# Kernel tuning notes

Hardware: AMD Instinct MI355X
Metric: run time of the kernel (lower is better)

The kernel has to match this reference:

```python
import jax, jax.numpy as jnp
import numpy as np

B, N, D, H = 2, 2048, 1024, 16
DH = D // H


def setup_inputs() -> dict:
    key = jax.random.key(0)
    ks = jax.random.split(key, 5)
    s = 0.02
    return {
        "x": jax.random.normal(ks[0], (B, N, D), dtype=jnp.float32),
        "Wq": jax.random.normal(ks[1], (D, D), dtype=jnp.float32) * s,
        "Wk": jax.random.normal(ks[2], (D, D), dtype=jnp.float32) * s,
        "Wv": jax.random.normal(ks[3], (D, D), dtype=jnp.float32) * s,
        "Wo": jax.random.normal(ks[4], (D, D), dtype=jnp.float32) * s,
        "bo": jnp.zeros((D,), dtype=jnp.float32),
    }


def reference(x, Wq, Wk, Wv, Wo, bo):
    b, n, d = x.shape
    # linear projections (torch Linear: y = x @ W.T), split into heads -> [b,h,n,dh]
    def proj(W):
        return jnp.einsum('bnd,ed->bne', x, W).reshape(b, n, H, DH).transpose(0, 2, 1, 3)
    q, k, v = proj(Wq), proj(Wk), proj(Wv)
    scores = jnp.einsum('bhqd,bhkd->bhqk', q, k)  # [b,h,n,n]
    causal = jnp.triu(jnp.ones((n, n), dtype=bool), k=1)
    scores = jnp.where(causal, -jnp.inf, scores)
    # NOTE: module scales by 1/sqrt(num_key_tokens), not 1/sqrt(d_head)
    w = jax.nn.softmax(scores / jnp.sqrt(jnp.float32(n)), axis=-1)
    ctx = jnp.einsum('bhqk,bhkd->bhqd', w, v)
    ctx = ctx.transpose(0, 2, 1, 3).reshape(b, n, d)
    return jnp.einsum('bnd,ed->bne', ctx, Wo) + bo
```

## Files before the change

### kernel.cpp

```cpp
#include <hip/hip_runtime.h>
#include <hip/hip_bf16.h>

typedef __attribute__((ext_vector_type(8))) short bf16x8;
typedef __attribute__((ext_vector_type(4))) float f32x4;
typedef __attribute__((ext_vector_type(16))) float f32x16;
typedef unsigned short u16;
typedef unsigned int u32;

__device__ __forceinline__ u16 f2bf(float f) {
  union { float f; unsigned int u; } v; v.f = f;
  return (u16)((v.u + 0x7fffu + ((v.u >> 16) & 1u)) >> 16);
}
__device__ __forceinline__ u32 pack_bf2(float f0, float f1) {
  union { float f; unsigned int u; } a, b; a.f = f0; b.f = f1;
  return __builtin_amdgcn_perm(b.u + 0x8000u, a.u + 0x8000u, 0x07060302u);
}

#define GLOAD_LDS16(g, l) __builtin_amdgcn_global_load_lds( \
    (const __attribute__((address_space(1))) void*)(g),     \
    (__attribute__((address_space(3))) void*)(l), 16, 0, 0)

__global__ __launch_bounds__(256) void conv_all(const float* __restrict__ x,
                                                const float* __restrict__ wq, const float* __restrict__ wk,
                                                const float* __restrict__ wv, const float* __restrict__ wo,
                                                u16* __restrict__ xb, u16* __restrict__ qo, u16* __restrict__ ko,
                                                u16* __restrict__ vo, u16* __restrict__ oo) {
  int y = blockIdx.y;
  const float* src; u16* dst;
  if (y < 4) { src = x + (size_t)y * 1048576; dst = xb + (size_t)y * 1048576; }
  else if (y == 4) { src = wq; dst = qo; }
  else if (y == 5) { src = wk; dst = ko; }
  else if (y == 6) { src = wv; dst = vo; }
  else { src = wo; dst = oo; }
  int i = (blockIdx.x * 256 + threadIdx.x) * 4;
  float4 v = *(const float4*)(src + i);
  ushort4 o;
  o.x = f2bf(v.x); o.y = f2bf(v.y); o.z = f2bf(v.z); o.w = f2bf(v.w);
  *(ushort4*)(dst + i) = o;
}

template <bool SW>
__device__ __forceinline__ void gemm_main(const u16* __restrict__ A, const u16* __restrict__ W,
                                          u16* As, u16* Bs, int m0, int n0, int K,
                                          f32x4 acc[4][4]) {
  int tid = threadIdx.x, wave = tid >> 6, lane = tid & 63;
  int lane15 = lane & 15, quad = lane >> 4;
  int wm = (wave >> 1) * 64, wn = (wave & 1) * 64;
  for (int k0 = 0; k0 < K; k0 += 64) {
    __syncthreads();
#pragma unroll
    for (int i = 0; i < 4; i++) {
      int rbase = wave * 32 + i * 8;
      int rloc = rbase + (lane >> 3);
      int ca = ((lane & 7) ^ (rloc & 7)) * 8;
      GLOAD_LDS16(A + (size_t)(m0 + rloc) * K + k0 + ca, As + rbase * 64);
      GLOAD_LDS16(W + (size_t)(n0 + rloc) * K + k0 + ca, Bs + rbase * 64);
    }
    __syncthreads();
#pragma unroll
    for (int kc = 0; kc < 2; kc++) {
      bf16x8 a[4], b[4];
#pragma unroll
      for (int mi = 0; mi < 4; mi++) {
        int m = wm + mi * 16 + lane15;
        a[mi] = *(const bf16x8*)(As + m * 64 + (((kc * 4 + quad) ^ (m & 7)) * 8));
      }
#pragma unroll
      for (int ni = 0; ni < 4; ni++) {
        int n = wn + ni * 16 + lane15;
        b[ni] = *(const bf16x8*)(Bs + n * 64 + (((kc * 4 + quad) ^ (n & 7)) * 8));
      }
#pragma unroll
      for (int mi = 0; mi < 4; mi++)
#pragma unroll
        for (int ni = 0; ni < 4; ni++)
          acc[mi][ni] = SW ? __builtin_amdgcn_mfma_f32_16x16x32_bf16(b[ni], a[mi], acc[mi][ni], 0, 0, 0)
                           : __builtin_amdgcn_mfma_f32_16x16x32_bf16(a[mi], b[ni], acc[mi][ni], 0, 0, 0);
    }
  }
}

__global__ __launch_bounds__(256, 3) void gemm_qkv(const u16* __restrict__ xb,
                                                   const u16* __restrict__ wq, const u16* __restrict__ wk,
                                                   const u16* __restrict__ wv,
                                                   u16* __restrict__ Qb, u16* __restrict__ Kb,
                                                   u16* __restrict__ Vtg) {
  __shared__ __align__(16) u16 As[128 * 64];
  __shared__ __align__(16) u16 Bs[128 * 64];
  const int K = 1024;
  int z = blockIdx.z;
  const u16* W = (z == 0) ? wq : (z == 1) ? wk : wv;
  int m0 = blockIdx.x * 128, n0 = blockIdx.y * 128;
  f32x4 acc[4][4];
#pragma unroll
  for (int i = 0; i < 4; i++)
#pragma unroll
    for (int j = 0; j < 4; j++) acc[i][j] = (f32x4){0.f, 0.f, 0.f, 0.f};

  int tid = threadIdx.x, wave = tid >> 6, lane = tid & 63;
  int lane15 = lane & 15, quad = lane >> 4;
  int wm = (wave >> 1) * 64, wn = (wave & 1) * 64;
  const float kQs = 0.022097086912079608f * 1.4426950408889634f;

  if (z < 2) {
    gemm_main<true>(xb, W, As, Bs, m0, n0, K, acc);
    u16* Out = z ? Kb : Qb;
    float sc = z ? 1.0f : kQs;
#pragma unroll
    for (int mi = 0; mi < 4; mi++)
#pragma unroll
      for (int ni = 0; ni < 4; ni++) {
        int token = m0 + wm + mi * 16 + lane15;
        int fb = n0 + wn + ni * 16 + quad * 4;
        ushort4 o;
        o.x = f2bf(acc[mi][ni][0] * sc); o.y = f2bf(acc[mi][ni][1] * sc);
        o.z = f2bf(acc[mi][ni][2] * sc); o.w = f2bf(acc[mi][ni][3] * sc);
        *(ushort4*)&Out[(size_t)token * 1024 + fb] = o;
      }
  } else {
    gemm_main<false>(xb, W, As, Bs, m0, n0, K, acc);
#pragma unroll
    for (int mi = 0; mi < 4; mi++)
#pragma unroll
      for (int ni = 0; ni < 4; ni++) {
        int row = m0 + wm + mi * 16 + quad * 4;
        int col = n0 + wn + ni * 16 + lane15;
        int bb = row >> 11, nn = row & 2047;
        ushort4 o;
        o.x = f2bf(acc[mi][ni][0]); o.y = f2bf(acc[mi][ni][1]);
        o.z = f2bf(acc[mi][ni][2]); o.w = f2bf(acc[mi][ni][3]);
        *(ushort4*)&Vtg[(size_t)(bb * 1024 + col) * 2048 + nn] = o;
      }
  }
}

__global__ __launch_bounds__(256, 2) void gemm_out(const u16* __restrict__ A, const u16* __restrict__ W,
                                                   float* __restrict__ Of, const float* __restrict__ bias) {
  __shared__ __align__(16) u16 As[128 * 64];
  __shared__ __align__(16) u16 Bs[64 * 64];
  const int K = 1024;
  int m0 = blockIdx.x * 128, n0 = blockIdx.y * 64;
  int tid = threadIdx.x, wave = tid >> 6, lane = tid & 63;
  int lane15 = lane & 15, quad = lane >> 4;
  int wm = (wave >> 1) * 64, wn = (wave & 1) * 32;
  f32x4 acc[4][2];
#pragma unroll
  for (int i = 0; i < 4; i++)
#pragma unroll
    for (int j = 0; j < 2; j++) acc[i][j] = (f32x4){0.f, 0.f, 0.f, 0.f};
  for (int k0 = 0; k0 < K; k0 += 64) {
    __syncthreads();
#pragma unroll
    for (int i = 0; i < 4; i++) {
      int rbase = wave * 32 + i * 8;
      int rloc = rbase + (lane >> 3);
      int ca = ((lane & 7) ^ (rloc & 7)) * 8;
      GLOAD_LDS16(A + (size_t)(m0 + rloc) * K + k0 + ca, As + rbase * 64);
    }
#pragma unroll
    for (int i = 0; i < 2; i++) {
      int rbase = wave * 16 + i * 8;
      int rloc = rbase + (lane >> 3);
      int ca = ((lane & 7) ^ (rloc & 7)) * 8;
      GLOAD_LDS16(W + (size_t)(n0 + rloc) * K + k0 + ca, Bs + rbase * 64);
    }
    __syncthreads();
#pragma unroll
    for (int kc = 0; kc < 2; kc++) {
      bf16x8 a[4], b[2];
#pragma unroll
      for (int mi = 0; mi < 4; mi++) {
        int m = wm + mi * 16 + lane15;
        a[mi] = *(const bf16x8*)(As + m * 64 + (((kc * 4 + quad) ^ (m & 7)) * 8));
      }
#pragma unroll
      for (int ni = 0; ni < 2; ni++) {
        int n = wn + ni * 16 + lane15;
        b[ni] = *(const bf16x8*)(Bs + n * 64 + (((kc * 4 + quad) ^ (n & 7)) * 8));
      }
#pragma unroll
      for (int mi = 0; mi < 4; mi++)
#pragma unroll
        for (int ni = 0; ni < 2; ni++)
          acc[mi][ni] = __builtin_amdgcn_mfma_f32_16x16x32_bf16(b[ni], a[mi], acc[mi][ni], 0, 0, 0);
    }
  }
#pragma unroll
  for (int mi = 0; mi < 4; mi++)
#pragma unroll
    for (int ni = 0; ni < 2; ni++) {
      int token = m0 + wm + mi * 16 + lane15;
      int fb = n0 + wn + ni * 16 + quad * 4;
      float4 bb = *(const float4*)&bias[fb];
      float4 o;
      o.x = acc[mi][ni][0] + bb.x; o.y = acc[mi][ni][1] + bb.y;
      o.z = acc[mi][ni][2] + bb.z; o.w = acc[mi][ni][3] + bb.w;
      *(float4*)&Of[(size_t)token * 1024 + fb] = o;
    }
}

__global__ __launch_bounds__(256, 4) void attn7(const u16* __restrict__ Q, const u16* __restrict__ Kg,
                                                const u16* __restrict__ Vtg, u16* __restrict__ ctx) {
  __shared__ __align__(16) u16 SH[16384];
  int tid = threadIdx.x, wave = tid >> 6, lane = tid & 63;
  int l31 = lane & 31, hf = lane >> 5;
  int qt = wave & 1, kvh = wave >> 1;

  int bh = blockIdx.x, by = blockIdx.y;
  int sidx = (by < 16) ? (31 - by) : (by - 16);
  int b = bh >> 4, h = bh & 15;
  int qbase = sidx * 64;

  bf16x8 qb[4];
#pragma unroll
  for (int s = 0; s < 4; s++)
    qb[s] = *(const bf16x8*)&Q[(size_t)(b * 2048 + qbase + qt * 32 + l31) * 1024 +
                               h * 64 + s * 16 + hf * 8];

  f32x16 oacc[2];
#pragma unroll
  for (int dt = 0; dt < 2; dt++)
#pragma unroll
    for (int r = 0; r < 16; r++) oacc[dt][r] = 0.f;
  float lsum = 0.f;

  auto stage = [&](int t, int d) {
    int tb = t * 64;
    u16* Kd = SH + d * 4096;
    u16* Vd = SH + 8192 + d * 4096;
#pragma unroll
    for (int i = 0; i < 2; i++) {
      int rbase = wave * 16 + i * 8;
      int rk = rbase + (lane >> 3);
      int ca = ((lane & 7) ^ (rk & 7)) * 8;
      GLOAD_LDS16(&Kg[(size_t)(b * 2048 + tb + rk) * 1024 + h * 64 + ca], Kd + rbase * 64);
      GLOAD_LDS16(&Vtg[(size_t)(b * 1024 + h * 64 + rk) * 2048 + tb + ca], Vd + rbase * 64);
    }
  };

  stage(0, 0);
  for (int t = 0; t <= sidx; ++t) {
    __syncthreads();
    if (t < sidx) stage(t + 1, (t + 1) & 1);
    int d = t & 1;
    const u16* Kd = SH + d * 4096;
    const u16* Vd = SH + 8192 + d * 4096;

    bool diag = (t == sidx);
    if (diag && kvh > qt) continue;

    int krow = kvh * 32 + l31;
    const u16* kp = Kd + krow * 64;
    bf16x8 kf[4];
#pragma unroll
    for (int s = 0; s < 4; s++)
      kf[s] = *(const bf16x8*)(kp + (((2 * s + hf) ^ (krow & 7)) * 8));

    f32x16 sv;
#pragma unroll
    for (int r = 0; r < 16; r++) sv[r] = 0.f;
#pragma unroll
    for (int s = 0; s < 4; s++)
      sv = __builtin_amdgcn_mfma_f32_32x32x16_bf16(kf[s], qb[s], sv, 0, 0, 0);

    if (diag && kvh == qt) {
#pragma unroll
      for (int r = 0; r < 16; r++) {
        int kvloc = (r & 3) + 8 * (r >> 2) + 4 * hf;
        if (kvloc > l31) sv[r] = -10000.0f;
      }
    }
#pragma unroll
    for (int r = 0; r < 16; r++) {
      float p = __builtin_amdgcn_exp2f(sv[r]);
      sv[r] = p; lsum += p;
    }
    u32 p0 = pack_bf2(sv[0], sv[1]),   p1 = pack_bf2(sv[2], sv[3]);
    u32 p2 = pack_bf2(sv[4], sv[5]),   p3 = pack_bf2(sv[6], sv[7]);
    u32 p4 = pack_bf2(sv[8], sv[9]),   p5 = pack_bf2(sv[10], sv[11]);
    u32 p6 = pack_bf2(sv[12], sv[13]), p7 = pack_bf2(sv[14], sv[15]);
    u32 x0 = __shfl_xor(hf ? p0 : p2, 32);
    u32 x1 = __shfl_xor(hf ? p1 : p3, 32);
    u32 x2 = __shfl_xor(hf ? p4 : p6, 32);
    u32 x3 = __shfl_xor(hf ? p5 : p7, 32);
    union U8 { u32 u[4]; bf16x8 v; };
    U8 pf0, pf1;
    pf0.u[0] = hf ? x0 : p0; pf0.u[1] = hf ? x1 : p1;
    pf0.u[2] = hf ? p2 : x0; pf0.u[3] = hf ? p3 : x1;
    pf1.u[0] = hf ? x2 : p4; pf1.u[1] = hf ? x3 : p5;
    pf1.u[2] = hf ? p6 : x2; pf1.u[3] = hf ? p7 : x3;

#pragma unroll
    for (int c = 0; c < 2; c++) {
      bf16x8 pf = c ? pf1.v : pf0.v;
#pragma unroll
      for (int dt = 0; dt < 2; dt++) {
        int vrow = dt * 32 + l31;
        bf16x8 va = *(const bf16x8*)(Vd + vrow * 64 + (((4 * kvh + 2 * c + hf) ^ (vrow & 7)) * 8));
        oacc[dt] = __builtin_amdgcn_mfma_f32_32x32x16_bf16(va, pf, oacc[dt], 0, 0, 0);
      }
    }
  }

  lsum += __shfl_xor(lsum, 32);
  float* MG = (float*)SH;
  float* LS = (float*)(SH + 8192);
  __syncthreads();
  if (kvh == 1) {
#pragma unroll
    for (int dt = 0; dt < 2; dt++) {
      float* p = MG + ((qt * 2 + dt) * 64 + lane) * 16;
#pragma unroll
      for (int gr = 0; gr < 4; gr++)
        *(f32x4*)(p + gr * 4) = (f32x4){oacc[dt][4 * gr], oacc[dt][4 * gr + 1],
                                        oacc[dt][4 * gr + 2], oacc[dt][4 * gr + 3]};
    }
    LS[qt * 32 + l31] = lsum;
  }
  __syncthreads();
  if (kvh == 0) {
    float inv = 1.0f / (lsum + LS[qt * 32 + l31]);
    int token = qbase + qt * 32 + l31;
    size_t off = (size_t)(b * 2048 + token) * 1024 + h * 64;
#pragma unroll
    for (int dt = 0; dt < 2; dt++) {
      const float* p = MG + ((qt * 2 + dt) * 64 + lane) * 16;
#pragma unroll
      for (int gr = 0; gr < 4; gr++) {
        f32x4 m = *(const f32x4*)(p + gr * 4);
        ushort4 o;
        o.x = f2bf((oacc[dt][4 * gr + 0] + m[0]) * inv);
        o.y = f2bf((oacc[dt][4 * gr + 1] + m[1]) * inv);
        o.z = f2bf((oacc[dt][4 * gr + 2] + m[2]) * inv);
        o.w = f2bf((oacc[dt][4 * gr + 3] + m[3]) * inv);
        *(ushort4*)&ctx[off + dt * 32 + 8 * gr + 4 * hf] = o;
      }
    }
  }
}

extern "C" void kernel_launch(void* const* d_in, const int* in_sizes, int n_in,
                              void* d_out, int out_size, void* d_ws, size_t ws_size,
                              hipStream_t stream) {
  const float* x  = (const float*)d_in[0];
  const float* Wq = (const float*)d_in[1];
  const float* Wk = (const float*)d_in[2];
  const float* Wv = (const float*)d_in[3];
  const float* Wo = (const float*)d_in[4];
  const float* bo = (const float*)d_in[5];
  float* out = (float*)d_out;
  char* ws = (char*)d_ws;
  const size_t MB = 1024 * 1024;
  u16* xb   = (u16*)(ws);
  u16* wqb  = (u16*)(ws +  8 * MB);
  u16* wkb  = (u16*)(ws + 10 * MB);
  u16* wvb  = (u16*)(ws + 12 * MB);
  u16* wob  = (u16*)(ws + 14 * MB);
  u16* Qb   = (u16*)(ws + 16 * MB);
  u16* Kb   = (u16*)(ws + 24 * MB);
  u16* Vtg  = (u16*)(ws + 32 * MB);
  u16* ctxb = (u16*)(ws + 40 * MB);

  conv_all<<<dim3(1024, 8), 256, 0, stream>>>(x, Wq, Wk, Wv, Wo, xb, wqb, wkb, wvb, wob);
  gemm_qkv<<<dim3(32, 8, 3), 256, 0, stream>>>(xb, wqb, wkb, wvb, Qb, Kb, Vtg);
  attn7<<<dim3(32, 32), 256, 0, stream>>>(Qb, Kb, Vtg, ctxb);
  gemm_out<<<dim3(32, 16), 256, 0, stream>>>(ctxb, wob, out, bo);
}
```

Before: 168.4 us.

## Widen attention query tile to 128 rows with per-wave full KV blocks

The attention kernel now gives each of the four waves its own 32 query rows, so a block covers 128 queries and every wave processes the full 64-key tile. Previously two waves split the keys and merged partial sums through shared memory. The change removes that cross-wave reduction and its extra barriers, halves the number of blocks, and doubles K/V reuse per staged tile. It also adds s_setprio around the MFMA sections. In exchange it raises register pressure (launch bounds drop to 2 blocks per CU), gives fewer blocks for load balance, and leaves waves idle on the diagonal tiles they skip.

```diff
diff --git a/kernel.cpp b/kernel.cpp
--- a/kernel.cpp
+++ b/kernel.cpp
@@ -199,23 +199,24 @@
     }
 }
 
-__global__ __launch_bounds__(256, 4) void attn7(const u16* __restrict__ Q, const u16* __restrict__ Kg,
+__global__ __launch_bounds__(256, 2) void attn8(const u16* __restrict__ Q, const u16* __restrict__ Kg,
                                                 const u16* __restrict__ Vtg, u16* __restrict__ ctx) {
   __shared__ __align__(16) u16 SH[16384];
   int tid = threadIdx.x, wave = tid >> 6, lane = tid & 63;
   int l31 = lane & 31, hf = lane >> 5;
-  int qt = wave & 1, kvh = wave >> 1;
+  int qt = wave;
 
   int bh = blockIdx.x, by = blockIdx.y;
-  int sidx = (by < 16) ? (31 - by) : (by - 16);
+  int sidx = (by < 8) ? (15 - by) : (by - 8);
   int b = bh >> 4, h = bh & 15;
-  int qbase = sidx * 64;
+  int qbase = sidx * 128;
+  int qw = qbase + qt * 32;
+  int gq = qw + l31;
 
   bf16x8 qb[4];
 #pragma unroll
   for (int s = 0; s < 4; s++)
-    qb[s] = *(const bf16x8*)&Q[(size_t)(b * 2048 + qbase + qt * 32 + l31) * 1024 +
-                               h * 64 + s * 16 + hf * 8];
+    qb[s] = *(const bf16x8*)&Q[(size_t)(b * 2048 + gq) * 1024 + h * 64 + s * 16 + hf * 8];
 
   f32x16 oacc[2];
 #pragma unroll
@@ -238,103 +239,111 @@
     }
   };
 
+  int tmax = 2 * sidx + 1;
   stage(0, 0);
-  for (int t = 0; t <= sidx; ++t) {
-    __syncthreads();
-    if (t < sidx) stage(t + 1, (t + 1) & 1);
+  for (int t = 0; t <= tmax; ++t) {
+    __syncthreads();
+    if (t < tmax) stage(t + 1, (t + 1) & 1);
+    if (t * 64 > qw + 31) continue;
     int d = t & 1;
     const u16* Kd = SH + d * 4096;
     const u16* Vd = SH + 8192 + d * 4096;
 
-    bool diag = (t == sidx);
-    if (diag && kvh > qt) continue;
-
-    int krow = kvh * 32 + l31;
-    const u16* kp = Kd + krow * 64;
-    bf16x8 kf[4];
-#pragma unroll
-    for (int s = 0; s < 4; s++)
-      kf[s] = *(const bf16x8*)(kp + (((2 * s + hf) ^ (krow & 7)) * 8));
-
-    f32x16 sv;
-#pragma unroll
-    for (int r = 0; r < 16; r++) sv[r] = 0.f;
-#pragma unroll
-    for (int s = 0; s < 4; s++)
-      sv = __builtin_amdgcn_mfma_f32_32x32x16_bf16(kf[s], qb[s], sv, 0, 0, 0);
-
-    if (diag && kvh == qt) {
+    const u16* kp0 = Kd + l31 * 64;
+    const u16* kp1 = Kd + (32 + l31) * 64;
+    bf16x8 kf0[4], kf1[4];
+#pragma unroll
+    for (int s = 0; s < 4; s++) {
+      int sw = ((2 * s + hf) ^ (l31 & 7)) * 8;
+      kf0[s] = *(const bf16x8*)(kp0 + sw);
+      kf1[s] = *(const bf16x8*)(kp1 + sw);
+    }
+
+    f32x16 sv0, sv1;
+#pragma unroll
+    for (int r = 0; r < 16; r++) { sv0[r] = 0.f; sv1[r] = 0.f; }
+    __builtin_amdgcn_s_setprio(1);
+#pragma unroll
+    for (int s = 0; s < 4; s++) {
+      sv0 = __builtin_amdgcn_mfma_f32_32x32x16_bf16(kf0[s], qb[s], sv0, 0, 0, 0);
+      sv1 = __builtin_amdgcn_mfma_f32_32x32x16_bf16(kf1[s], qb[s], sv1, 0, 0, 0);
+    }
+    __builtin_amdgcn_s_setprio(0);
+
+    if (t * 64 + 63 > qw) {
 #pragma unroll
       for (int r = 0; r < 16; r++) {
-        int kvloc = (r & 3) + 8 * (r >> 2) + 4 * hf;
-        if (kvloc > l31) sv[r] = -10000.0f;
+        int kv = t * 64 + (r & 3) + 8 * (r >> 2) + 4 * hf;
+        if (kv > gq) sv0[r] = -10000.0f;
+        if (kv + 32 > gq) sv1[r] = -10000.0f;
       }
     }
 #pragma unroll
     for (int r = 0; r < 16; r++) {
-      float p = __builtin_amdgcn_exp2f(sv[r]);
-      sv[r] = p; lsum += p;
-    }
-    u32 p0 = pack_bf2(sv[0], sv[1]),   p1 = pack_bf2(sv[2], sv[3]);
-    u32 p2 = pack_bf2(sv[4], sv[5]),   p3 = pack_bf2(sv[6], sv[7]);
-    u32 p4 = pack_bf2(sv[8], sv[9]),   p5 = pack_bf2(sv[10], sv[11]);
-    u32 p6 = pack_bf2(sv[12], sv[13]), p7 = pack_bf2(sv[14], sv[15]);
-    u32 x0 = __shfl_xor(hf ? p0 : p2, 32);
-    u32 x1 = __shfl_xor(hf ? p1 : p3, 32);
-    u32 x2 = __shfl_xor(hf ? p4 : p6, 32);
-    u32 x3 = __shfl_xor(hf ? p5 : p7, 32);
+      float p = __builtin_amdgcn_exp2f(sv0[r]); sv0[r] = p; lsum += p;
+    }
+#pragma unroll
+    for (int r = 0; r < 16; r++) {
+      float p = __builtin_amdgcn_exp2f(sv1[r]); sv1[r] = p; lsum += p;
+    }
+
     union U8 { u32 u[4]; bf16x8 v; };
-    U8 pf0, pf1;
-    pf0.u[0] = hf ? x0 : p0; pf0.u[1] = hf ? x1 : p1;
-    pf0.u[2] = hf ? p2 : x0; pf0.u[3] = hf ? p3 : x1;
-    pf1.u[0] = hf ? x2 : p4; pf1.u[1] = hf ? x3 : p5;
-    pf1.u[2] = hf ? p6 : x2; pf1.u[3] = hf ? p7 : x3;
-
-#pragma unroll
-    for (int c = 0; c < 2; c++) {
-      bf16x8 pf = c ? pf1.v : pf0.v;
+    U8 pf[4];
+    {
+      u32 p0 = pack_bf2(sv0[0], sv0[1]),   p1 = pack_bf2(sv0[2], sv0[3]);
+      u32 p2 = pack_bf2(sv0[4], sv0[5]),   p3 = pack_bf2(sv0[6], sv0[7]);
+      u32 p4 = pack_bf2(sv0[8], sv0[9]),   p5 = pack_bf2(sv0[10], sv0[11]);
+      u32 p6 = pack_bf2(sv0[12], sv0[13]), p7 = pack_bf2(sv0[14], sv0[15]);
+      u32 x0 = __shfl_xor(hf ? p0 : p2, 32);
+      u32 x1 = __shfl_xor(hf ? p1 : p3, 32);
+      u32 x2 = __shfl_xor(hf ? p4 : p6, 32);
+      u32 x3 = __shfl_xor(hf ? p5 : p7, 32);
+      pf[0].u[0] = hf ? x0 : p0; pf[0].u[1] = hf ? x1 : p1;
+      pf[0].u[2] = hf ? p2 : x0; pf[0].u[3] = hf ? p3 : x1;
+      pf[1].u[0] = hf ? x2 : p4; pf[1].u[1] = hf ? x3 : p5;
+      pf[1].u[2] = hf ? p6 : x2; pf[1].u[3] = hf ? p7 : x3;
+    }
+    {
+      u32 p0 = pack_bf2(sv1[0], sv1[1]),   p1 = pack_bf2(sv1[2], sv1[3]);
+      u32 p2 = pack_bf2(sv1[4], sv1[5]),   p3 = pack_bf2(sv1[6], sv1[7]);
+      u32 p4 = pack_bf2(sv1[8], sv1[9]),   p5 = pack_bf2(sv1[10], sv1[11]);
+      u32 p6 = pack_bf2(sv1[12], sv1[13]), p7 = pack_bf2(sv1[14], sv1[15]);
+      u32 x0 = __shfl_xor(hf ? p0 : p2, 32);
+      u32 x1 = __shfl_xor(hf ? p1 : p3, 32);
+      u32 x2 = __shfl_xor(hf ? p4 : p6, 32);
+      u32 x3 = __shfl_xor(hf ? p5 : p7, 32);
+      pf[2].u[0] = hf ? x0 : p0; pf[2].u[1] = hf ? x1 : p1;
+      pf[2].u[2] = hf ? p2 : x0; pf[2].u[3] = hf ? p3 : x1;
+      pf[3].u[0] = hf ? x2 : p4; pf[3].u[1] = hf ? x3 : p5;
+      pf[3].u[2] = hf ? p6 : x2; pf[3].u[3] = hf ? p7 : x3;
+    }
+
+    __builtin_amdgcn_s_setprio(1);
+#pragma unroll
+    for (int c = 0; c < 4; c++) {
 #pragma unroll
       for (int dt = 0; dt < 2; dt++) {
         int vrow = dt * 32 + l31;
-        bf16x8 va = *(const bf16x8*)(Vd + vrow * 64 + (((4 * kvh + 2 * c + hf) ^ (vrow & 7)) * 8));
-        oacc[dt] = __builtin_amdgcn_mfma_f32_32x32x16_bf16(va, pf, oacc[dt], 0, 0, 0);
-      }
-    }
+        bf16x8 va = *(const bf16x8*)(Vd + vrow * 64 + (((2 * c + hf) ^ (vrow & 7)) * 8));
+        oacc[dt] = __builtin_amdgcn_mfma_f32_32x32x16_bf16(va, pf[c].v, oacc[dt], 0, 0, 0);
+      }
+    }
+    __builtin_amdgcn_s_setprio(0);
   }
 
   lsum += __shfl_xor(lsum, 32);
-  float* MG = (float*)SH;
-  float* LS = (float*)(SH + 8192);
-  __syncthreads();
-  if (kvh == 1) {
-#pragma unroll
-    for (int dt = 0; dt < 2; dt++) {
-      float* p = MG + ((qt * 2 + dt) * 64 + lane) * 16;
-#pragma unroll
-      for (int gr = 0; gr < 4; gr++)
-        *(f32x4*)(p + gr * 4) = (f32x4){oacc[dt][4 * gr], oacc[dt][4 * gr + 1],
-                                        oacc[dt][4 * gr + 2], oacc[dt][4 * gr + 3]};
-    }
-    LS[qt * 32 + l31] = lsum;
-  }
-  __syncthreads();
-  if (kvh == 0) {
-    float inv = 1.0f / (lsum + LS[qt * 32 + l31]);
-    int token = qbase + qt * 32 + l31;
-    size_t off = (size_t)(b * 2048 + token) * 1024 + h * 64;
-#pragma unroll
-    for (int dt = 0; dt < 2; dt++) {
-      const float* p = MG + ((qt * 2 + dt) * 64 + lane) * 16;
-#pragma unroll
-      for (int gr = 0; gr < 4; gr++) {
-        f32x4 m = *(const f32x4*)(p + gr * 4);
-        ushort4 o;
-        o.x = f2bf((oacc[dt][4 * gr + 0] + m[0]) * inv);
-        o.y = f2bf((oacc[dt][4 * gr + 1] + m[1]) * inv);
-        o.z = f2bf((oacc[dt][4 * gr + 2] + m[2]) * inv);
-        o.w = f2bf((oacc[dt][4 * gr + 3] + m[3]) * inv);
-        *(ushort4*)&ctx[off + dt * 32 + 8 * gr + 4 * hf] = o;
-      }
+  float inv = 1.0f / lsum;
+  size_t off = (size_t)(b * 2048 + gq) * 1024 + h * 64;
+#pragma unroll
+  for (int dt = 0; dt < 2; dt++) {
+#pragma unroll
+    for (int gr = 0; gr < 4; gr++) {
+      ushort4 o;
+      o.x = f2bf(oacc[dt][4 * gr + 0] * inv);
+      o.y = f2bf(oacc[dt][4 * gr + 1] * inv);
+      o.z = f2bf(oacc[dt][4 * gr + 2] * inv);
+      o.w = f2bf(oacc[dt][4 * gr + 3] * inv);
+      *(ushort4*)&ctx[off + dt * 32 + 8 * gr + 4 * hf] = o;
     }
   }
 }
@@ -363,6 +372,6 @@
 
   conv_all<<<dim3(1024, 8), 256, 0, stream>>>(x, Wq, Wk, Wv, Wo, xb, wqb, wkb, wvb, wob);
   gemm_qkv<<<dim3(32, 8, 3), 256, 0, stream>>>(xb, wqb, wkb, wvb, Qb, Kb, Vtg);
-  attn7<<<dim3(32, 32), 256, 0, stream>>>(Qb, Kb, Vtg, ctxb);
+  attn8<<<dim3(32, 16), 256, 0, stream>>>(Qb, Kb, Vtg, ctxb);
   gemm_out<<<dim3(32, 16), 256, 0, stream>>>(ctxb, wob, out, bo);
 }
```

Measured after the change: 169.5 us. No clear change (+0.6%).
